# Kernel optimization log

Hardware: AMD Instinct MI355X
Metric: run time of the kernel (lower is better)

Reference implementation:

```python
import jax, jax.numpy as jnp
import numpy as np

DIM = 384
HEADS = 6
HEAD_DIM = DIM // HEADS
SCALE = HEAD_DIM ** -0.5


def setup_inputs() -> dict:
    key = jax.random.key(0)
    k1, k2, k3, k4, k5 = jax.random.split(key, 5)
    B, N, C = 2, 4096, DIM
    x = jax.random.normal(k1, (B, N, C), dtype=jnp.float32)
    mask = jax.random.randint(k2, (B, N), 0, 2) > 0  # bool [B, N]
    w_qkv = jax.random.normal(k3, (3 * C, C), dtype=jnp.float32) * (C ** -0.5)
    w_proj = jax.random.normal(k4, (C, C), dtype=jnp.float32) * (C ** -0.5)
    b_proj = jax.random.normal(k5, (C,), dtype=jnp.float32) * 0.01
    return {"x": x, "mask": mask, "w_qkv": w_qkv, "w_proj": w_proj, "b_proj": b_proj}


def reference(x, mask, w_qkv, w_proj, b_proj):
    B, N, C = x.shape
    # qkv projection (no bias), split into q, k, v of shape [B, H, N, hd]
    qkv = (x @ w_qkv.T).reshape(B, N, 3, HEADS, HEAD_DIM).transpose(2, 0, 3, 1, 4)
    q, k, v = qkv[0], qkv[1], qkv[2]
    attn = jnp.einsum('bhqd,bhkd->bhqk', q, k) * SCALE  # [B, H, N, N]
    # pairwise mask: mask[:, None, :] * mask[:, :, None], broadcast over heads
    pair = (mask[:, None, :, None] & mask[:, None, None, :])  # [B, 1, N, N]
    neg = -jnp.finfo(attn.dtype).max
    attn = jnp.where(pair, attn, neg)
    attn = jax.nn.softmax(attn, axis=-1)
    out = jnp.einsum('bhqk,bhkd->bhqd', attn, v)  # [B, H, N, hd]
    out = out.transpose(0, 2, 1, 3).reshape(B, N, C)
    return out @ w_proj.T + b_proj
```

## Files before the change

### kernel.cpp

```cpp
#include <hip/hip_runtime.h>
#include <cfloat>
#include <cstdint>
#include <cstddef>

using u16 = unsigned short;
typedef __attribute__((ext_vector_type(8))) short short8;
typedef __attribute__((ext_vector_type(4))) float f32x4;

#define HEADS 6
#define NSEQ 4096
#define SCALEF 0.125f
#define LOG2E 1.4426950408889634f
#define SC2 (SCALEF * LOG2E)

#if __has_builtin(__builtin_amdgcn_exp2f)
#define EXP2(x) __builtin_amdgcn_exp2f(x)
#else
#define EXP2(x) exp2f(x)
#endif

__device__ __forceinline__ u16 f2bf_rn(float f) {
  unsigned int u = __builtin_bit_cast(unsigned int, f);
  u = (u + 0x7FFFu + ((u >> 16) & 1u)) >> 16;
  return (u16)u;
}

__device__ __forceinline__ void gload_lds16(const void* g, void* l) {
  __builtin_amdgcn_global_load_lds((const __attribute__((address_space(1))) void*)g,
                                   (__attribute__((address_space(3))) void*)l, 16, 0, 0);
}

__device__ __forceinline__ short8 frag_read(const u16* tile, int row, int blk) {
  int byt = row * 128 + ((blk * 16) ^ ((row & 7) << 4));
  return *(const short8*)((const char*)tile + byt);
}

__device__ __forceinline__ void cast8(const float* __restrict__ s, u16* __restrict__ d, int i) {
  const float4* sp = (const float4*)s;
  float4 a = sp[2 * i], b = sp[2 * i + 1];
  short8 r;
  r[0] = (short)f2bf_rn(a.x); r[1] = (short)f2bf_rn(a.y);
  r[2] = (short)f2bf_rn(a.z); r[3] = (short)f2bf_rn(a.w);
  r[4] = (short)f2bf_rn(b.x); r[5] = (short)f2bf_rn(b.y);
  r[6] = (short)f2bf_rn(b.z); r[7] = (short)f2bf_rn(b.w);
  ((short8*)d)[i] = r;
}

__global__ void prep_kernel(const float* __restrict__ x, const float* __restrict__ wqkv,
                            const float* __restrict__ wproj, const int* __restrict__ mask,
                            u16* __restrict__ xb, u16* __restrict__ wqb, u16* __restrict__ wpb,
                            float* __restrict__ madd,
                            int* __restrict__ cpos, float* __restrict__ acm, int* __restrict__ nth) {
  __shared__ int cnt[256];
  __shared__ int offu[256];
  __shared__ int s_nc;
  const int NX = 3145728 / 8, NQ = 442368 / 8, NP = 147456 / 8;
  const int NPREP_BLK = 1856;
  if (blockIdx.x >= NPREP_BLK) {
    int b = blockIdx.x - NPREP_BLK;
    int t = threadIdx.x;
    const int* m = mask + b * NSEQ;
    int base = t * 16;
    int c = 0;
#pragma unroll
    for (int i = 0; i < 16; ++i) c += (m[base + i] != 0) ? 1 : 0;
    cnt[t] = c;
    __syncthreads();
    if (t == 0) {
      int s = 0;
      for (int i = 0; i < 256; ++i) { offu[i] = s; s += cnt[i]; }
      s_nc = s;
      int ncpad = (s + 127) & ~127;
      if (ncpad == 0) ncpad = 128;
      nth[b] = ncpad / 128;
    }
    __syncthreads();
    int nc = s_nc;
    int ou = offu[t];
    int om = base - ou;
    for (int i = 0; i < 16; ++i) {
      int n = base + i;
      int um = (m[n] != 0) ? 1 : 0;
      int pos = um ? ou : (nc + om);
      ou += um;
      om += 1 - um;
      cpos[b * NSEQ + n] = pos;
      acm[b * NSEQ + pos] = um ? 0.f : -FLT_MAX;
    }
    return;
  }
  int i = blockIdx.x * blockDim.x + threadIdx.x;
  if (i < NX) cast8(x, xb, i);
  else if (i < NX + NQ) cast8(wqkv, wqb, i - NX);
  else if (i < NX + NQ + NP) cast8(wproj, wpb, i - NX - NQ);
  else {
    int j = i - (NX + NQ + NP);
    if (j < 2 * NSEQ) madd[j] = mask[j] ? 0.f : -FLT_MAX;
  }
}

__global__ void meanv_kernel(const u16* __restrict__ vt, float* __restrict__ meanv) {
  int row = blockIdx.x;
  const u16* src = vt + (size_t)row * NSEQ + threadIdx.x * 8;
  float s = 0.f;
#pragma unroll
  for (int i = 0; i < 8; ++i) {
    short8 v = *(const short8*)(src + i * 512);
#pragma unroll
    for (int j = 0; j < 8; ++j) {
      unsigned int u = ((unsigned int)(unsigned short)v[j]) << 16;
      s += __builtin_bit_cast(float, u);
    }
  }
#pragma unroll
  for (int off = 1; off < 64; off <<= 1) s += __shfl_xor(s, off);
  if (threadIdx.x == 0) meanv[row] = s * (1.0f / NSEQ);
}

template <int EPI>
__launch_bounds__(256)
__global__ void gemm_bt(const u16* __restrict__ A, const u16* __restrict__ B,
                        int Kdim, int Ndim,
                        u16* __restrict__ q_out, u16* __restrict__ k_out, u16* __restrict__ vt_out,
                        const int* __restrict__ cpos,
                        const float* __restrict__ bias, float* __restrict__ out) {
  __shared__ u16 lA[128 * 64];
  __shared__ u16 lB[128 * 64];
  int brow = blockIdx.x, bcol = blockIdx.y;
  int tid = threadIdx.x;
  int w = tid >> 6, lane = tid & 63;
  int wr = w >> 1, wc = w & 1;
  int r_in = lane >> 3;
  int jblk = (lane & 7) ^ r_in;
  int l15 = lane & 15, lg = lane >> 4;

  f32x4 acc[4][4];
#pragma unroll
  for (int i = 0; i < 4; i++)
#pragma unroll
    for (int j = 0; j < 4; j++) acc[i][j] = (f32x4){0.f, 0.f, 0.f, 0.f};

  const u16* Ab = A + (size_t)(brow * 128 + w * 32 + r_in) * Kdim + jblk * 8;
  const u16* Bb = B + (size_t)(bcol * 128 + w * 32 + r_in) * Kdim + jblk * 8;

  int ksteps = Kdim >> 6;
  for (int kt = 0; kt < ksteps; ++kt) {
    __syncthreads();
#pragma unroll
    for (int c = 0; c < 4; ++c) {
      gload_lds16(Ab + kt * 64 + (size_t)(c * 8) * Kdim, &lA[(w * 32 + c * 8) * 64]);
      gload_lds16(Bb + kt * 64 + (size_t)(c * 8) * Kdim, &lB[(w * 32 + c * 8) * 64]);
    }
    asm volatile("s_waitcnt vmcnt(0)" ::: "memory");
    __syncthreads();

    short8 af[4][2], bfr[4][2];
#pragma unroll
    for (int ms = 0; ms < 4; ++ms)
#pragma unroll
      for (int hf = 0; hf < 2; ++hf)
        af[ms][hf] = frag_read(lA, wr * 64 + ms * 16 + l15, hf * 4 + lg);
#pragma unroll
    for (int ns = 0; ns < 4; ++ns)
#pragma unroll
      for (int hf = 0; hf < 2; ++hf)
        bfr[ns][hf] = frag_read(lB, wc * 64 + ns * 16 + l15, hf * 4 + lg);
#pragma unroll
    for (int ms = 0; ms < 4; ++ms)
#pragma unroll
      for (int ns = 0; ns < 4; ++ns) {
        acc[ms][ns] = __builtin_amdgcn_mfma_f32_16x16x32_bf16(af[ms][0], bfr[ns][0], acc[ms][ns], 0, 0, 0);
        acc[ms][ns] = __builtin_amdgcn_mfma_f32_16x16x32_bf16(af[ms][1], bfr[ns][1], acc[ms][ns], 0, 0, 0);
      }
  }

#pragma unroll
  for (int ms = 0; ms < 4; ++ms)
#pragma unroll
    for (int ns = 0; ns < 4; ++ns)
#pragma unroll
      for (int r = 0; r < 4; ++r) {
        int row_g = brow * 128 + wr * 64 + ms * 16 + lg * 4 + r;
        int col_g = bcol * 128 + wc * 64 + ns * 16 + l15;
        float v = acc[ms][ns][r];
        if (EPI == 0) {
          int t = col_g / 384;
          int rem = col_g - t * 384;
          int h = rem >> 6, d = rem & 63;
          int b = row_g >> 12;
          u16 val = f2bf_rn(v);
          size_t bh = (size_t)(b * HEADS + h);
          int pp = cpos[row_g];
          if (t == 0)      q_out[(bh * NSEQ + pp) * 64 + d] = val;
          else if (t == 1) k_out[(bh * NSEQ + pp) * 64 + d] = val;
          else             vt_out[(bh * 64 + d) * NSEQ + pp] = val;
        } else {
          out[(size_t)row_g * Ndim + col_g] = v + bias[col_g];
        }
      }
}

template <int KS>
__launch_bounds__(256, 3)
__global__ void attn_kernel32(const u16* __restrict__ qg, const u16* __restrict__ kg,
                              const u16* __restrict__ vtg,
                              const float* __restrict__ acm, const int* __restrict__ nth,
                              float* __restrict__ o_part, float* __restrict__ l_part) {
  __shared__ u16 lK[2][64 * 64];
  __shared__ u16 lV[2][64 * 64];

  int bid = blockIdx.x;
  int orig = (bid & 7) * (48 * KS) + (bid >> 3);
  int qb = orig & 31;
  int rr = orig >> 5;
  int bh = rr % 12, kh = rr / 12;

  int b = bh / HEADS;
  const int nt_b = nth[b];
  if (qb >= nt_b) return;
  int kt_total = nt_b * 2;
  int st = (kh * kt_total) / KS;
  int NTL = ((kh + 1) * kt_total) / KS - st;
  int kbase = st * 64;

  int tid = threadIdx.x;
  int w = tid >> 6, lane = tid & 63;
  int l15 = lane & 15, lg = lane >> 4;
  int r_in = lane >> 3, jblk = (lane & 7) ^ r_in;

  const u16* Q = qg + (size_t)bh * NSEQ * 64;
  const u16* K = kg + (size_t)bh * NSEQ * 64;
  const u16* VT = vtg + (size_t)bh * 64 * NSEQ;
  const float* acrow = acm + b * NSEQ;

  int q0 = qb * 128 + w * 32;
  int qrow0 = q0 + l15, qrow1 = q0 + 16 + l15;
  short8 qfA[2], qfB[2];
#pragma unroll
  for (int hf = 0; hf < 2; ++hf) {
    qfA[hf] = *(const short8*)(Q + (size_t)qrow0 * 64 + hf * 32 + lg * 8);
    qfB[hf] = *(const short8*)(Q + (size_t)qrow1 * 64 + hf * 32 + lg * 8);
  }

  float qsel0 = (acrow[qrow0] == 0.0f) ? 1.0f : 0.0f;
  float qsel1 = (acrow[qrow1] == 0.0f) ? 1.0f : 0.0f;
  float scq0 = SC2 * qsel0, scq1 = SC2 * qsel1;

  int swk = (l15 & 7) << 4;
  int offKA = l15 * 128 + ((lg * 16) ^ swk);
  int offKB = l15 * 128 + (((4 + lg) * 16) ^ swk);

  f32x4 acc0[4], acc1[4];
#pragma unroll
  for (int ds_ = 0; ds_ < 4; ++ds_) {
    acc0[ds_] = (f32x4){0.f, 0.f, 0.f, 0.f};
    acc1[ds_] = (f32x4){0.f, 0.f, 0.f, 0.f};
  }
  f32x4 lsum0 = (f32x4){0.f, 0.f, 0.f, 0.f};
  f32x4 lsum1 = (f32x4){0.f, 0.f, 0.f, 0.f};

#define STAGE(BUF, k0s)                                                                     \
  {                                                                                         \
    _Pragma("unroll")                                                                       \
    for (int c = 0; c < 2; ++c) {                                                           \
      int rowb = w * 16 + c * 8;                                                            \
      gload_lds16(K + (size_t)((k0s) + rowb + r_in) * 64 + jblk * 8, &lK[BUF][rowb * 64]);  \
      gload_lds16(VT + (size_t)(rowb + r_in) * NSEQ + (k0s) + jblk * 8, &lV[BUF][rowb * 64]);\
    }                                                                                       \
  }

  if (NTL > 0) {
    STAGE(0, kbase);
    asm volatile("s_waitcnt vmcnt(0)" ::: "memory");
    __syncthreads();

    int cur = 0;
    for (int t = 0; t < NTL; ++t) {
      if (t + 1 < NTL) STAGE(cur ^ 1, kbase + (t + 1) * 64);

      const char* kb = (const char*)lK[cur];
      const char* vb = (const char*)lV[cur];

      f32x4 p0[4], p1[4];
      __builtin_amdgcn_s_setprio(1);
#pragma unroll
      for (int cs = 0; cs < 4; ++cs) {
        short8 kf0 = *(const short8*)(kb + offKA + cs * 2048);
        short8 kf1 = *(const short8*)(kb + offKB + cs * 2048);
        f32x4 z0 = (f32x4){0.f, 0.f, 0.f, 0.f};
        f32x4 z1 = (f32x4){0.f, 0.f, 0.f, 0.f};
        z0 = __builtin_amdgcn_mfma_f32_16x16x32_bf16(kf0, qfA[0], z0, 0, 0, 0);
        z1 = __builtin_amdgcn_mfma_f32_16x16x32_bf16(kf0, qfB[0], z1, 0, 0, 0);
        p0[cs] = __builtin_amdgcn_mfma_f32_16x16x32_bf16(kf1, qfA[1], z0, 0, 0, 0);
        p1[cs] = __builtin_amdgcn_mfma_f32_16x16x32_bf16(kf1, qfB[1], z1, 0, 0, 0);
      }
      __builtin_amdgcn_s_setprio(0);

      int k0 = kbase + t * 64;
#pragma unroll
      for (int cs = 0; cs < 4; ++cs) {
        f32x4 mf = *(const f32x4*)(acrow + k0 + cs * 16 + lg * 4);
        f32x4 d0 = p0[cs] * scq0 + mf * qsel0;
        f32x4 d1 = p1[cs] * scq1 + mf * qsel1;
#pragma unroll
        for (int r = 0; r < 4; ++r) {
          p0[cs][r] = EXP2(d0[r]);
          p1[cs][r] = EXP2(d1[r]);
        }
      }
      lsum0 += (p0[0] + p0[1]) + (p0[2] + p0[3]);
      lsum1 += (p1[0] + p1[1]) + (p1[2] + p1[3]);

      short8 pfA[2], pfB[2];
      {
        uint32_t wd[4][2];
#pragma unroll
        for (int cs = 0; cs < 4; ++cs)
#pragma unroll
          for (int hh = 0; hh < 2; ++hh)
            asm("v_cvt_pk_bf16_f32 %0, %1, %2" : "=v"(wd[cs][hh]) : "v"(p0[cs][2 * hh]), "v"(p0[cs][2 * hh + 1]));
#pragma unroll
        for (int c = 0; c < 2; ++c) {
          union { uint32_t u[4]; short8 s8; } cv;
#pragma unroll
          for (int hh = 0; hh < 2; ++hh) {
            uint32_t A = wd[2 * c][hh], B = wd[2 * c + 1][hh];
            asm("v_permlane32_swap_b32 %0, %1" : "+v"(A), "+v"(B));
            asm("v_permlane16_swap_b32 %0, %1" : "+v"(A), "+v"(B));
            cv.u[hh] = A;
            cv.u[2 + hh] = B;
          }
          pfA[c] = cv.s8;
        }
      }
      {
        uint32_t wd[4][2];
#pragma unroll
        for (int cs = 0; cs < 4; ++cs)
#pragma unroll
          for (int hh = 0; hh < 2; ++hh)
            asm("v_cvt_pk_bf16_f32 %0, %1, %2" : "=v"(wd[cs][hh]) : "v"(p1[cs][2 * hh]), "v"(p1[cs][2 * hh + 1]));
#pragma unroll
        for (int c = 0; c < 2; ++c) {
          union { uint32_t u[4]; short8 s8; } cv;
#pragma unroll
          for (int hh = 0; hh < 2; ++hh) {
            uint32_t A = wd[2 * c][hh], B = wd[2 * c + 1][hh];
            asm("v_permlane32_swap_b32 %0, %1" : "+v"(A), "+v"(B));
            asm("v_permlane16_swap_b32 %0, %1" : "+v"(A), "+v"(B));
            cv.u[hh] = A;
            cv.u[2 + hh] = B;
          }
          pfB[c] = cv.s8;
        }
      }

      __builtin_amdgcn_s_setprio(1);
#pragma unroll
      for (int ds_ = 0; ds_ < 4; ++ds_) {
        short8 vf0 = *(const short8*)(vb + offKA + ds_ * 2048);
        short8 vf1 = *(const short8*)(vb + offKB + ds_ * 2048);
        acc0[ds_] = __builtin_amdgcn_mfma_f32_16x16x32_bf16(vf0, pfA[0], acc0[ds_], 0, 0, 0);
        acc0[ds_] = __builtin_amdgcn_mfma_f32_16x16x32_bf16(vf1, pfA[1], acc0[ds_], 0, 0, 0);
        acc1[ds_] = __builtin_amdgcn_mfma_f32_16x16x32_bf16(vf0, pfB[0], acc1[ds_], 0, 0, 0);
        acc1[ds_] = __builtin_amdgcn_mfma_f32_16x16x32_bf16(vf1, pfB[1], acc1[ds_], 0, 0, 0);
      }
      __builtin_amdgcn_s_setprio(0);

      __syncthreads();
      cur ^= 1;
    }
  }

  float rsum0 = (lsum0[0] + lsum0[1]) + (lsum0[2] + lsum0[3]);
  rsum0 += __shfl_xor(rsum0, 16);
  rsum0 += __shfl_xor(rsum0, 32);
  float rsum1 = (lsum1[0] + lsum1[1]) + (lsum1[2] + lsum1[3]);
  rsum1 += __shfl_xor(rsum1, 16);
  rsum1 += __shfl_xor(rsum1, 32);

  float* op = o_part + (size_t)kh * (8192ull * 384);
  int hd = bh - b * HEADS;
  size_t base0 = ((size_t)b * NSEQ + qrow0) * 384 + hd * 64;
  size_t base1 = ((size_t)b * NSEQ + qrow1) * 384 + hd * 64;
#pragma unroll
  for (int ds_ = 0; ds_ < 4; ++ds_) {
    *(f32x4*)(op + base0 + ds_ * 16 + lg * 4) = acc0[ds_];
    *(f32x4*)(op + base1 + ds_ * 16 + lg * 4) = acc1[ds_];
  }
  if (lg == 0) {
    l_part[(kh * 12 + bh) * NSEQ + qrow0] = rsum0;
    l_part[(kh * 12 + bh) * NSEQ + qrow1] = rsum1;
  }
#undef STAGE
}

template <int KS>
__global__ void combine_kernel(const float* __restrict__ o_part, const float* __restrict__ l_part,
                               const float* __restrict__ madd, const float* __restrict__ meanv,
                               const int* __restrict__ cpos, u16* __restrict__ out) {
  int i = blockIdx.x * blockDim.x + threadIdx.x;
  int elem = i * 4;
  int ng = elem / 384;
  int cc = elem - ng * 384;
  int h = cc >> 6, d = cc & 63;
  int b = ng >> 12;

  float a0, a1, a2, a3;
  if (madd[ng] != 0.0f) {
    const float* mv = meanv + (b * HEADS + h) * 64 + d;
    a0 = mv[0]; a1 = mv[1]; a2 = mv[2]; a3 = mv[3];
  } else {
    int pos = cpos[ng];
    size_t pbase = (size_t)(b * NSEQ + pos) * 384 + cc;
    int li = (b * HEADS + h) * NSEQ + pos;
    float4 a = *(const float4*)(o_part + pbase);
    float lt = l_part[li];
#pragma unroll
    for (int kh = 1; kh < KS; ++kh) {
      float4 c = *(const float4*)(o_part + (size_t)kh * (8192ull * 384) + pbase);
      a.x += c.x; a.y += c.y; a.z += c.z; a.w += c.w;
      lt += l_part[kh * 12 * NSEQ + li];
    }
    float inv = 1.0f / lt;
    a0 = a.x * inv; a1 = a.y * inv; a2 = a.z * inv; a3 = a.w * inv;
  }
  uint32_t w0, w1;
  asm("v_cvt_pk_bf16_f32 %0, %1, %2" : "=v"(w0) : "v"(a0), "v"(a1));
  asm("v_cvt_pk_bf16_f32 %0, %1, %2" : "=v"(w1) : "v"(a2), "v"(a3));
  uint2 st; st.x = w0; st.y = w1;
  *(uint2*)(out + elem) = st;
}

extern "C" void kernel_launch(void* const* d_in, const int* in_sizes, int n_in,
                              void* d_out, int out_size, void* d_ws, size_t ws_size,
                              hipStream_t stream) {
  const float* x = (const float*)d_in[0];
  const int* mask = (const int*)d_in[1];
  const float* w_qkv = (const float*)d_in[2];
  const float* w_proj = (const float*)d_in[3];
  const float* b_proj = (const float*)d_in[4];
  float* out = (float*)d_out;

  char* ws = (char*)d_ws;
  u16* x_bf = (u16*)(ws + 0);
  u16* wqkv_bf = (u16*)(ws + 6291456);
  u16* wproj_bf = (u16*)(ws + 7176192);
  u16* q_bf = (u16*)(ws + 7471104);
  u16* k_bf = (u16*)(ws + 13762560);
  u16* vt_bf = (u16*)(ws + 20054016);
  u16* attn_bf = (u16*)(ws + 26345472);
  float* madd = (float*)(ws + 32636928);
  int* cpos = (int*)(ws + 32669696);
  float* acm = (float*)(ws + 32702464);
  int* nth = (int*)(ws + 32735232);
  float* meanv = (float*)(ws + 32735296);
  float* o_part = (float*)(ws + 32738432);

  const int NPREP_GRID = 1856 + 2;
  prep_kernel<<<NPREP_GRID, 256, 0, stream>>>(x, w_qkv, w_proj, mask,
                                              x_bf, wqkv_bf, wproj_bf, madd,
                                              cpos, acm, nth);

  gemm_bt<0><<<dim3(64, 9), 256, 0, stream>>>(x_bf, wqkv_bf, 384, 1152,
                                              q_bf, k_bf, vt_bf, cpos, nullptr, nullptr);

  meanv_kernel<<<768, 64, 0, stream>>>(vt_bf, meanv);

  if (ws_size >= 32738432ull + 4ull * 12582912 + 4ull * 196608) {
    float* l_part = (float*)(ws + 32738432 + 4ull * 12582912);
    attn_kernel32<4><<<1536, 256, 0, stream>>>(q_bf, k_bf, vt_bf, acm, nth, o_part, l_part);
    combine_kernel<4><<<3072, 256, 0, stream>>>(o_part, l_part, madd, meanv, cpos, attn_bf);
  } else {
    float* l_part = (float*)(ws + 32738432 + 2ull * 12582912);
    attn_kernel32<2><<<768, 256, 0, stream>>>(q_bf, k_bf, vt_bf, acm, nth, o_part, l_part);
    combine_kernel<2><<<3072, 256, 0, stream>>>(o_part, l_part, madd, meanv, cpos, attn_bf);
  }

  gemm_bt<1><<<dim3(64, 3), 256, 0, stream>>>(attn_bf, wproj_bf, 384, 384,
                                              nullptr, nullptr, nullptr, nullptr, b_proj, out);
}
```

Before: 93.09 us.

## Single-buffer K/V tiles in attention for higher occupancy and add KS=8 split

After: 210.9 us. 127% more time.

```diff
diff --git a/kernel.cpp b/kernel.cpp
--- a/kernel.cpp
+++ b/kernel.cpp
@@ -201,13 +201,13 @@
 }
 
 template <int KS>
-__launch_bounds__(256, 3)
+__launch_bounds__(256, 6)
 __global__ void attn_kernel32(const u16* __restrict__ qg, const u16* __restrict__ kg,
                               const u16* __restrict__ vtg,
                               const float* __restrict__ acm, const int* __restrict__ nth,
                               float* __restrict__ o_part, float* __restrict__ l_part) {
-  __shared__ u16 lK[2][64 * 64];
-  __shared__ u16 lV[2][64 * 64];
+  __shared__ u16 lK[64 * 64];
+  __shared__ u16 lV[64 * 64];
 
   int bid = blockIdx.x;
   int orig = (bid & 7) * (48 * KS) + (bid >> 3);
@@ -259,27 +259,24 @@
   f32x4 lsum0 = (f32x4){0.f, 0.f, 0.f, 0.f};
   f32x4 lsum1 = (f32x4){0.f, 0.f, 0.f, 0.f};
 
-#define STAGE(BUF, k0s)                                                                     \
-  {                                                                                         \
-    _Pragma("unroll")                                                                       \
-    for (int c = 0; c < 2; ++c) {                                                           \
-      int rowb = w * 16 + c * 8;                                                            \
-      gload_lds16(K + (size_t)((k0s) + rowb + r_in) * 64 + jblk * 8, &lK[BUF][rowb * 64]);  \
-      gload_lds16(VT + (size_t)(rowb + r_in) * NSEQ + (k0s) + jblk * 8, &lV[BUF][rowb * 64]);\
-    }                                                                                       \
+#define STAGE(k0s)                                                                      \
+  {                                                                                     \
+    _Pragma("unroll")                                                                   \
+    for (int c = 0; c < 2; ++c) {                                                       \
+      int rowb = w * 16 + c * 8;                                                        \
+      gload_lds16(K + (size_t)((k0s) + rowb + r_in) * 64 + jblk * 8, &lK[rowb * 64]);   \
+      gload_lds16(VT + (size_t)(rowb + r_in) * NSEQ + (k0s) + jblk * 8, &lV[rowb * 64]);\
+    }                                                                                   \
   }
 
   if (NTL > 0) {
-    STAGE(0, kbase);
+    STAGE(kbase);
     asm volatile("s_waitcnt vmcnt(0)" ::: "memory");
     __syncthreads();
 
-    int cur = 0;
     for (int t = 0; t < NTL; ++t) {
-      if (t + 1 < NTL) STAGE(cur ^ 1, kbase + (t + 1) * 64);
-
-      const char* kb = (const char*)lK[cur];
-      const char* vb = (const char*)lV[cur];
+      const char* kb = (const char*)lK;
+      const char* vb = (const char*)lV;
 
       f32x4 p0[4], p1[4];
       __builtin_amdgcn_s_setprio(1);
@@ -368,7 +365,11 @@
       __builtin_amdgcn_s_setprio(0);
 
       __syncthreads();
-      cur ^= 1;
+      if (t + 1 < NTL) {
+        STAGE(kbase + (t + 1) * 64);
+        asm volatile("s_waitcnt vmcnt(0)" ::: "memory");
+        __syncthreads();
+      }
     }
   }
 
@@ -467,7 +468,13 @@
 
   meanv_kernel<<<768, 64, 0, stream>>>(vt_bf, meanv);
 
-  if (ws_size >= 32738432ull + 4ull * 12582912 + 4ull * 196608) {
+  const size_t WS_KS8 = 32738432ull + 8ull * 12582912 + 8ull * 196608;
+  const size_t WS_KS4 = 32738432ull + 4ull * 12582912 + 4ull * 196608;
+  if (ws_size >= WS_KS8) {
+    float* l_part = (float*)(ws + 32738432 + 8ull * 12582912);
+    attn_kernel32<8><<<3072, 256, 0, stream>>>(q_bf, k_bf, vt_bf, acm, nth, o_part, l_part);
+    combine_kernel<8><<<3072, 256, 0, stream>>>(o_part, l_part, madd, meanv, cpos, attn_bf);
+  } else if (ws_size >= WS_KS4) {
     float* l_part = (float*)(ws + 32738432 + 4ull * 12582912);
     attn_kernel32<4><<<1536, 256, 0, stream>>>(q_bf, k_bf, vt_bf, acm, nth, o_part, l_part);
     combine_kernel<4><<<3072, 256, 0, stream>>>(o_part, l_part, madd, meanv, cpos, attn_bf);
```
